# Kernel optimization log

Measured on AMD Instinct MI355X. Metric: run time of the kernel, lower is better.

The kernel has to match this reference:

```python
import jax, jax.numpy as jnp
import numpy as np

N = 8192
E = 262144


def gconv(x, e0, e1, W, b):
    # Dense symmetric adjacency with set-to-1 semantics (duplicates collapse),
    # matching adj[e0,e1]=1; adj[e1,e0]=1 in the original.
    n = x.shape[0]
    adj = jnp.zeros((n, n), x.dtype).at[e0, e1].set(1.0).at[e1, e0].set(1.0)
    adj = adj + jnp.eye(n, dtype=x.dtype)  # self-loops (selfloop=True branch)
    deg = jnp.sum(adj, axis=1)
    dinv = 1.0 / jnp.sqrt(deg)
    # D @ adj @ D expressed as row/col scaling (same math, no O(n^3) diag matmuls)
    adj = dinv[:, None] * adj * dinv[None, :]
    return adj @ (x @ W) + b


def setup_inputs() -> dict:
    key = jax.random.key(0)
    ks = jax.random.split(key, 8)
    x = jax.random.normal(ks[0], (N, 512), dtype=jnp.float32)
    edge_index = jax.random.randint(ks[1], (2, E), 0, N, dtype=jnp.int64)
    W1 = jax.random.normal(ks[2], (512, 512), dtype=jnp.float32)
    b1 = jnp.zeros((512,), dtype=jnp.float32)
    W2 = jax.random.normal(ks[3], (512, 512), dtype=jnp.float32)
    b2 = jnp.zeros((512,), dtype=jnp.float32)
    W3 = jax.random.normal(ks[4], (512, 256), dtype=jnp.float32)
    b3 = jnp.zeros((256,), dtype=jnp.float32)
    return {"x": x, "edge_index": edge_index, "W1": W1, "b1": b1,
            "W2": W2, "b2": b2, "W3": W3, "b3": b3}


def reference(x, edge_index, W1, b1, W2, b2, W3, b3):
    e0, e1 = edge_index[0], edge_index[1]
    # eval mode: dropout_edge / dropout are identity; norm=False so no PairNorm
    h = jax.nn.relu(gconv(x, e0, e1, W1, b1))   # conv1: inputs -> wide
    h = jax.nn.relu(gconv(h, e0, e1, W2, b2))   # conv2: blocks=3 -> one middle layer
    out = gconv(h, e0, e1, W3, b3)              # conv3: wide -> outputs
    return out
```

## Files before the change

### kernel.cpp

```cpp
#include <hip/hip_runtime.h>
#include <stdint.h>

#define NN 8192
#define WPR 256
#define CSTRIDE 192

typedef _Float16 f16;
typedef f16 f16x2 __attribute__((ext_vector_type(2)));
typedef f16 f16x4 __attribute__((ext_vector_type(4)));
typedef f16 f16x8 __attribute__((ext_vector_type(8)));
typedef float f32x4 __attribute__((ext_vector_type(4)));

__global__ __launch_bounds__(256) void build_adj(const int* __restrict__ ei,
                                                 uint32_t* __restrict__ mask,
                                                 int E) {
  int t = blockIdx.x * blockDim.x + threadIdx.x;
  if (t >= E) return;
  int a = ei[t];
  int b = ei[E + t];
  atomicOr(&mask[(size_t)a * WPR + (b >> 5)], 1u << (b & 31));
  atomicOr(&mask[(size_t)b * WPR + (a >> 5)], 1u << (a & 31));
}

__global__ __launch_bounds__(256) void mask_to_csr(const uint32_t* __restrict__ mask,
                                                   uint16_t* __restrict__ cols,
                                                   int* __restrict__ nnz,
                                                   float* __restrict__ dinv) {
  const int row = blockIdx.x * 4 + (threadIdx.x >> 6);
  const int lane = threadIdx.x & 63;
  const uint4 w = ((const uint4*)(mask + (size_t)row * WPR))[lane];
  const int c = __popc(w.x) + __popc(w.y) + __popc(w.z) + __popc(w.w);
  int inc = c;
#pragma unroll
  for (int o = 1; o < 64; o <<= 1) {
    int v = __shfl_up(inc, o);
    if (lane >= o) inc += v;
  }
  const int total = __shfl(inc, 63);
  int base = row * CSTRIDE + (inc - c);
  const int lim = row * CSTRIDE + CSTRIDE;
  uint32_t ws_[4] = {w.x, w.y, w.z, w.w};
#pragma unroll
  for (int i = 0; i < 4; ++i) {
    uint32_t word = ws_[i];
    int boff = (lane * 4 + i) << 5;
    while (word) {
      int b = __ffs(word) - 1;
      word &= word - 1;
      if (base < lim) cols[base] = (uint16_t)(boff + b);
      ++base;
    }
  }
  if (lane == 0) {
    nnz[row] = (total > CSTRIDE) ? CSTRIDE : total;
    dinv[row] = rsqrtf((float)(total + 1));
  }
}

__global__ __launch_bounds__(256) void wcvt_all(const float* __restrict__ W1,
                                                const float* __restrict__ W2,
                                                const float* __restrict__ W3,
                                                f16* __restrict__ T1,
                                                f16* __restrict__ T2,
                                                f16* __restrict__ T3) {
  int tile = blockIdx.x;
  const float* W; f16* T; int N;
  if (tile < 256)      { W = W1; T = T1; N = 512; }
  else if (tile < 512) { W = W2; T = T2; N = 512; tile -= 256; }
  else                 { W = W3; T = T3; N = 256; tile -= 512; }
  const int K = 512;
  const int ntn = N >> 5;
  const int k0 = (tile / ntn) << 5, n0 = (tile % ntn) << 5;
  __shared__ f16 tl[32][33];
  const int tx = threadIdx.x & 31, ty = threadIdx.x >> 5;
#pragma unroll
  for (int r = 0; r < 32; r += 8)
    tl[ty + r][tx] = (f16)W[(size_t)(k0 + ty + r) * N + n0 + tx];
  __syncthreads();
#pragma unroll
  for (int r = 0; r < 32; r += 8)
    T[(size_t)(n0 + ty + r) * K + k0 + tx] = tl[tx][ty + r];
}

template <typename AT>
__global__ __launch_bounds__(256) void gemm_f16(const AT* __restrict__ A,
                                                const f16* __restrict__ Wt,
                                                const float* __restrict__ rs,
                                                f16* __restrict__ Ys,
                                                int M, int N, int K) {
  __shared__ f16 As[128][40];
  __shared__ f16 Bs[64][40];
  const int t = threadIdx.x;
  const int lane = t & 63;
  const int w = t >> 6;
  const int wr = w >> 1, wc = w & 1;
  const int m0 = blockIdx.y * 128, n0 = blockIdx.x * 64;
  const int lm = lane & 15, kg = lane >> 4;
  const int k0f = kg * 8;

  f32x4 acc[4][2] = {};

  for (int k0 = 0; k0 < K; k0 += 32) {
    if constexpr (sizeof(AT) == 4) {
#pragma unroll
      for (int l = 0; l < 4; ++l) {
        int row = (t >> 3) + l * 32;
        int c4 = (t & 7) * 4;
        float4 v = *(const float4*)&A[(size_t)(m0 + row) * K + k0 + c4];
        f16x4 h = {(f16)v.x, (f16)v.y, (f16)v.z, (f16)v.w};
        *(f16x4*)&As[row][c4] = h;
      }
    } else {
#pragma unroll
      for (int l = 0; l < 2; ++l) {
        int idx = l * 256 + t;
        int row = idx >> 2;
        int c8 = (idx & 3) * 8;
        f16x8 h = *(const f16x8*)&A[(size_t)(m0 + row) * K + k0 + c8];
        *(f16x8*)&As[row][c8] = h;
      }
    }
    {
      int n = t >> 2, k8 = (t & 3) * 8;
      *(f16x8*)&Bs[n][k8] = *(const f16x8*)&Wt[(size_t)(n0 + n) * K + k0 + k8];
    }
    __syncthreads();

    f16x8 af[4], bf[2];
#pragma unroll
    for (int mf = 0; mf < 4; ++mf)
      af[mf] = *(const f16x8*)&As[wr * 64 + mf * 16 + lm][k0f];
#pragma unroll
    for (int nf = 0; nf < 2; ++nf)
      bf[nf] = *(const f16x8*)&Bs[wc * 32 + nf * 16 + lm][k0f];
#pragma unroll
    for (int mf = 0; mf < 4; ++mf)
#pragma unroll
      for (int nf = 0; nf < 2; ++nf)
        acc[mf][nf] = __builtin_amdgcn_mfma_f32_16x16x32_f16(af[mf], bf[nf], acc[mf][nf], 0, 0, 0);
    __syncthreads();
  }

#pragma unroll
  for (int mf = 0; mf < 4; ++mf) {
#pragma unroll
    for (int r = 0; r < 4; ++r) {
      int row = m0 + wr * 64 + mf * 16 + kg * 4 + r;
      float s = rs[row];
#pragma unroll
      for (int nf = 0; nf < 2; ++nf) {
        int col = n0 + wc * 32 + nf * 16 + lm;
        Ys[(size_t)row * N + col] = (f16)(s * acc[mf][nf][r]);
      }
    }
  }
}

template <int NC, typename OutT, bool RELU>
__global__ __launch_bounds__(256) void spmm_csr(const uint16_t* __restrict__ cols,
                                                const int* __restrict__ nnz,
                                                const float* __restrict__ dinv,
                                                const f16* __restrict__ Ys,
                                                const float* __restrict__ bias,
                                                OutT* __restrict__ out) {
  constexpr int Q = NC / 128;
  const int b = blockIdx.x;
  const int chunk = b % Q;
  const int rg = b / Q;
  const int w = threadIdx.x >> 6, lane = threadIdx.x & 63;
  const int row = rg * 4 + w;
  const int cb = chunk * 128 + 2 * lane;

  __shared__ uint16_t cidx[4][CSTRIDE];
  const int n = nnz[row];
  for (int k = lane; k < n; k += 64) cidx[w][k] = cols[row * CSTRIDE + k];
  __syncthreads();

  const f16* __restrict__ Yc = Ys + cb;
  float a0 = 0.f, a1 = 0.f;
  int k = 0;
  for (; k + 16 <= n; k += 16) {
    f16x2 v0  = *(const f16x2*)&Yc[(size_t)cidx[w][k + 0]  * NC];
    f16x2 v1  = *(const f16x2*)&Yc[(size_t)cidx[w][k + 1]  * NC];
    f16x2 v2  = *(const f16x2*)&Yc[(size_t)cidx[w][k + 2]  * NC];
    f16x2 v3  = *(const f16x2*)&Yc[(size_t)cidx[w][k + 3]  * NC];
    f16x2 v4  = *(const f16x2*)&Yc[(size_t)cidx[w][k + 4]  * NC];
    f16x2 v5  = *(const f16x2*)&Yc[(size_t)cidx[w][k + 5]  * NC];
    f16x2 v6  = *(const f16x2*)&Yc[(size_t)cidx[w][k + 6]  * NC];
    f16x2 v7  = *(const f16x2*)&Yc[(size_t)cidx[w][k + 7]  * NC];
    f16x2 v8  = *(const f16x2*)&Yc[(size_t)cidx[w][k + 8]  * NC];
    f16x2 v9  = *(const f16x2*)&Yc[(size_t)cidx[w][k + 9]  * NC];
    f16x2 v10 = *(const f16x2*)&Yc[(size_t)cidx[w][k + 10] * NC];
    f16x2 v11 = *(const f16x2*)&Yc[(size_t)cidx[w][k + 11] * NC];
    f16x2 v12 = *(const f16x2*)&Yc[(size_t)cidx[w][k + 12] * NC];
    f16x2 v13 = *(const f16x2*)&Yc[(size_t)cidx[w][k + 13] * NC];
    f16x2 v14 = *(const f16x2*)&Yc[(size_t)cidx[w][k + 14] * NC];
    f16x2 v15 = *(const f16x2*)&Yc[(size_t)cidx[w][k + 15] * NC];
    f16x2 s0 = ((v0 + v1) + (v2 + v3)) + ((v4 + v5) + (v6 + v7));
    f16x2 s1 = ((v8 + v9) + (v10 + v11)) + ((v12 + v13) + (v14 + v15));
    a0 += (float)s0[0] + (float)s1[0];
    a1 += (float)s0[1] + (float)s1[1];
  }
  for (; k + 8 <= n; k += 8) {
    f16x2 v0 = *(const f16x2*)&Yc[(size_t)cidx[w][k + 0] * NC];
    f16x2 v1 = *(const f16x2*)&Yc[(size_t)cidx[w][k + 1] * NC];
    f16x2 v2 = *(const f16x2*)&Yc[(size_t)cidx[w][k + 2] * NC];
    f16x2 v3 = *(const f16x2*)&Yc[(size_t)cidx[w][k + 3] * NC];
    f16x2 v4 = *(const f16x2*)&Yc[(size_t)cidx[w][k + 4] * NC];
    f16x2 v5 = *(const f16x2*)&Yc[(size_t)cidx[w][k + 5] * NC];
    f16x2 v6 = *(const f16x2*)&Yc[(size_t)cidx[w][k + 6] * NC];
    f16x2 v7 = *(const f16x2*)&Yc[(size_t)cidx[w][k + 7] * NC];
    f16x2 s = ((v0 + v1) + (v2 + v3)) + ((v4 + v5) + (v6 + v7));
    a0 += (float)s[0];
    a1 += (float)s[1];
  }
  for (; k < n; ++k) {
    f16x2 v = *(const f16x2*)&Yc[(size_t)cidx[w][k] * NC];
    a0 += (float)v[0]; a1 += (float)v[1];
  }
  f16x2 vs = *(const f16x2*)&Yc[(size_t)row * NC];
  a0 += (float)vs[0]; a1 += (float)vs[1];
  const float di = dinv[row];
  float o0 = di * a0 + bias[cb];
  float o1 = di * a1 + bias[cb + 1];
  if (RELU) { o0 = fmaxf(o0, 0.f); o1 = fmaxf(o1, 0.f); }
  if constexpr (sizeof(OutT) == 4) {
    *(float2*)&out[(size_t)row * NC + cb] = make_float2(o0, o1);
  } else {
    f16x2 h = {(f16)o0, (f16)o1};
    *(f16x2*)&out[(size_t)row * NC + cb] = h;
  }
}

extern "C" void kernel_launch(void* const* d_in, const int* in_sizes, int n_in,
                              void* d_out, int out_size, void* d_ws, size_t ws_size,
                              hipStream_t stream) {
  const float* x  = (const float*)d_in[0];
  const int*   ei = (const int*)d_in[1];
  const float* W1 = (const float*)d_in[2];
  const float* b1 = (const float*)d_in[3];
  const float* W2 = (const float*)d_in[4];
  const float* b2 = (const float*)d_in[5];
  const float* W3 = (const float*)d_in[6];
  const float* b3 = (const float*)d_in[7];
  float* out = (float*)d_out;
  const int E = in_sizes[1] / 2;

  uint8_t* ws = (uint8_t*)d_ws;
  size_t off = 0;
  uint16_t* cols = (uint16_t*)ws;            off += (size_t)CSTRIDE * NN * 2;
  int*      nnz  = (int*)(ws + off);         off += (size_t)NN * 4;
  float*    dinv = (float*)(ws + off);       off += (size_t)NN * 4;
  f16*      Wt1  = (f16*)(ws + off);         off += (size_t)512 * 512 * 2;
  f16*      Wt2  = (f16*)(ws + off);         off += (size_t)512 * 512 * 2;
  f16*      Wt3  = (f16*)(ws + off);         off += (size_t)256 * 512 * 2;
  f16*      H    = (f16*)(ws + off);         off += (size_t)NN * 512 * 2;
  f16*      Ys   = (f16*)(ws + off);
  uint32_t* mask = (uint32_t*)Ys;

  hipMemsetAsync(mask, 0, (size_t)NN * WPR * sizeof(uint32_t), stream);
  build_adj<<<(E + 255) / 256, 256, 0, stream>>>(ei, mask, E);
  mask_to_csr<<<NN / 4, 256, 0, stream>>>(mask, cols, nnz, dinv);
  wcvt_all<<<640, 256, 0, stream>>>(W1, W2, W3, Wt1, Wt2, Wt3);

  gemm_f16<float><<<dim3(8, 64), 256, 0, stream>>>(x, Wt1, dinv, Ys, NN, 512, 512);
  spmm_csr<512, f16, true><<<(NN / 4) * 4, 256, 0, stream>>>(cols, nnz, dinv, Ys, b1, H);

  gemm_f16<f16><<<dim3(8, 64), 256, 0, stream>>>(H, Wt2, dinv, Ys, NN, 512, 512);
  spmm_csr<512, f16, true><<<(NN / 4) * 4, 256, 0, stream>>>(cols, nnz, dinv, Ys, b2, H);

  gemm_f16<f16><<<dim3(4, 64), 256, 0, stream>>>(H, Wt3, dinv, Ys, NN, 256, 512);
  spmm_csr<256, float, false><<<(NN / 4) * 2, 256, 0, stream>>>(cols, nnz, dinv, Ys, b3, out);
}
```

Measured before the change: 223.2 us.

## Replace tiled GEMM with full-K panel GEMM and pre-convert x to fp16

The GEMM now loads a 32-row by full-K A panel into shared memory once, and each wave streams its slice of the transposed weights directly from global/L2 with no per-k-step barriers. Each block covers every output column, so A is read only once. The fp32 input x is converted to fp16 up front inside the weight-prep kernel, so all three GEMMs share one fp16 code path. The cost is an extra pass over x, 32KB of LDS per block, and B fragments that come from cache rather than shared memory. It also increases per-wave accumulator registers.

New measurement: 235.1 us. +5.3%, slower.

```diff
diff --git a/kernel.cpp b/kernel.cpp
--- a/kernel.cpp
+++ b/kernel.cpp
@@ -57,13 +57,24 @@
   }
 }
 
-__global__ __launch_bounds__(256) void wcvt_all(const float* __restrict__ W1,
+__global__ __launch_bounds__(256) void prep_all(const float* __restrict__ W1,
                                                 const float* __restrict__ W2,
                                                 const float* __restrict__ W3,
+                                                const float* __restrict__ x,
                                                 f16* __restrict__ T1,
                                                 f16* __restrict__ T2,
-                                                f16* __restrict__ T3) {
+                                                f16* __restrict__ T3,
+                                                f16* __restrict__ Xh) {
   int tile = blockIdx.x;
+  if (tile >= 640) {
+    size_t base = (size_t)(tile - 640) * 2048 + threadIdx.x * 8;
+    float4 v0 = *(const float4*)&x[base];
+    float4 v1 = *(const float4*)&x[base + 4];
+    f16x8 h = {(f16)v0.x, (f16)v0.y, (f16)v0.z, (f16)v0.w,
+               (f16)v1.x, (f16)v1.y, (f16)v1.z, (f16)v1.w};
+    *(f16x8*)&Xh[base] = h;
+    return;
+  }
   const float* W; f16* T; int N;
   if (tile < 256)      { W = W1; T = T1; N = 512; }
   else if (tile < 512) { W = W2; T = T2; N = 512; tile -= 256; }
@@ -82,74 +93,55 @@
     T[(size_t)(n0 + ty + r) * K + k0 + tx] = tl[tx][ty + r];
 }
 
-template <typename AT>
-__global__ __launch_bounds__(256) void gemm_f16(const AT* __restrict__ A,
-                                                const f16* __restrict__ Wt,
-                                                const float* __restrict__ rs,
-                                                f16* __restrict__ Ys,
-                                                int M, int N, int K) {
-  __shared__ f16 As[128][40];
-  __shared__ f16 Bs[64][40];
+template <int N>
+__global__ __launch_bounds__(256) void gemm_panel(const f16* __restrict__ A,
+                                                  const f16* __restrict__ Wt,
+                                                  const float* __restrict__ rs,
+                                                  f16* __restrict__ Ys) {
+  constexpr int K = 512;
+  constexpr int NF = N / 64;
+  __shared__ f16 As[32 * K];
   const int t = threadIdx.x;
   const int lane = t & 63;
   const int w = t >> 6;
-  const int wr = w >> 1, wc = w & 1;
-  const int m0 = blockIdx.y * 128, n0 = blockIdx.x * 64;
   const int lm = lane & 15, kg = lane >> 4;
-  const int k0f = kg * 8;
-
-  f32x4 acc[4][2] = {};
-
+  const int m0 = blockIdx.x * 32;
+  const int n0w = w * (N / 4);
+
+#pragma unroll
+  for (int i = 0; i < 8; ++i) {
+    int idx = i * 256 + t;
+    *(f16x8*)&As[idx * 8] = *(const f16x8*)&A[(size_t)m0 * K + idx * 8];
+  }
+  __syncthreads();
+
+  f32x4 acc[2][NF] = {};
+#pragma unroll 4
   for (int k0 = 0; k0 < K; k0 += 32) {
-    if constexpr (sizeof(AT) == 4) {
-#pragma unroll
-      for (int l = 0; l < 4; ++l) {
-        int row = (t >> 3) + l * 32;
-        int c4 = (t & 7) * 4;
-        float4 v = *(const float4*)&A[(size_t)(m0 + row) * K + k0 + c4];
-        f16x4 h = {(f16)v.x, (f16)v.y, (f16)v.z, (f16)v.w};
-        *(f16x4*)&As[row][c4] = h;
-      }
-    } else {
-#pragma unroll
-      for (int l = 0; l < 2; ++l) {
-        int idx = l * 256 + t;
-        int row = idx >> 2;
-        int c8 = (idx & 3) * 8;
-        f16x8 h = *(const f16x8*)&A[(size_t)(m0 + row) * K + k0 + c8];
-        *(f16x8*)&As[row][c8] = h;
-      }
-    }
-    {
-      int n = t >> 2, k8 = (t & 3) * 8;
-      *(f16x8*)&Bs[n][k8] = *(const f16x8*)&Wt[(size_t)(n0 + n) * K + k0 + k8];
-    }
-    __syncthreads();
-
-    f16x8 af[4], bf[2];
-#pragma unroll
-    for (int mf = 0; mf < 4; ++mf)
-      af[mf] = *(const f16x8*)&As[wr * 64 + mf * 16 + lm][k0f];
-#pragma unroll
-    for (int nf = 0; nf < 2; ++nf)
-      bf[nf] = *(const f16x8*)&Bs[wc * 32 + nf * 16 + lm][k0f];
-#pragma unroll
-    for (int mf = 0; mf < 4; ++mf)
-#pragma unroll
-      for (int nf = 0; nf < 2; ++nf)
+    f16x8 af[2];
+#pragma unroll
+    for (int mf = 0; mf < 2; ++mf)
+      af[mf] = *(const f16x8*)&As[(mf * 16 + lm) * K + k0 + kg * 8];
+    f16x8 bf[NF];
+#pragma unroll
+    for (int nf = 0; nf < NF; ++nf)
+      bf[nf] = *(const f16x8*)&Wt[(size_t)(n0w + nf * 16 + lm) * K + k0 + kg * 8];
+#pragma unroll
+    for (int mf = 0; mf < 2; ++mf)
+#pragma unroll
+      for (int nf = 0; nf < NF; ++nf)
         acc[mf][nf] = __builtin_amdgcn_mfma_f32_16x16x32_f16(af[mf], bf[nf], acc[mf][nf], 0, 0, 0);
-    __syncthreads();
-  }
-
-#pragma unroll
-  for (int mf = 0; mf < 4; ++mf) {
+  }
+
+#pragma unroll
+  for (int mf = 0; mf < 2; ++mf) {
 #pragma unroll
     for (int r = 0; r < 4; ++r) {
-      int row = m0 + wr * 64 + mf * 16 + kg * 4 + r;
+      int row = m0 + mf * 16 + kg * 4 + r;
       float s = rs[row];
 #pragma unroll
-      for (int nf = 0; nf < 2; ++nf) {
-        int col = n0 + wc * 32 + nf * 16 + lm;
+      for (int nf = 0; nf < NF; ++nf) {
+        int col = n0w + nf * 16 + lm;
         Ys[(size_t)row * N + col] = (f16)(s * acc[mf][nf][r]);
       }
     }
@@ -254,6 +246,7 @@
   f16*      Wt1  = (f16*)(ws + off);         off += (size_t)512 * 512 * 2;
   f16*      Wt2  = (f16*)(ws + off);         off += (size_t)512 * 512 * 2;
   f16*      Wt3  = (f16*)(ws + off);         off += (size_t)256 * 512 * 2;
+  f16*      Xh   = (f16*)(ws + off);         off += (size_t)NN * 512 * 2;
   f16*      H    = (f16*)(ws + off);         off += (size_t)NN * 512 * 2;
   f16*      Ys   = (f16*)(ws + off);
   uint32_t* mask = (uint32_t*)Ys;
@@ -261,14 +254,14 @@
   hipMemsetAsync(mask, 0, (size_t)NN * WPR * sizeof(uint32_t), stream);
   build_adj<<<(E + 255) / 256, 256, 0, stream>>>(ei, mask, E);
   mask_to_csr<<<NN / 4, 256, 0, stream>>>(mask, cols, nnz, dinv);
-  wcvt_all<<<640, 256, 0, stream>>>(W1, W2, W3, Wt1, Wt2, Wt3);
-
-  gemm_f16<float><<<dim3(8, 64), 256, 0, stream>>>(x, Wt1, dinv, Ys, NN, 512, 512);
+  prep_all<<<2688, 256, 0, stream>>>(W1, W2, W3, x, Wt1, Wt2, Wt3, Xh);
+
+  gemm_panel<512><<<NN / 32, 256, 0, stream>>>(Xh, Wt1, dinv, Ys);
   spmm_csr<512, f16, true><<<(NN / 4) * 4, 256, 0, stream>>>(cols, nnz, dinv, Ys, b1, H);
 
-  gemm_f16<f16><<<dim3(8, 64), 256, 0, stream>>>(H, Wt2, dinv, Ys, NN, 512, 512);
+  gemm_panel<512><<<NN / 32, 256, 0, stream>>>(H, Wt2, dinv, Ys);
   spmm_csr<512, f16, true><<<(NN / 4) * 4, 256, 0, stream>>>(cols, nnz, dinv, Ys, b2, H);
 
-  gemm_f16<f16><<<dim3(4, 64), 256, 0, stream>>>(H, Wt3, dinv, Ys, NN, 256, 512);
+  gemm_panel<256><<<NN / 32, 256, 0, stream>>>(H, Wt3, dinv, Ys);
   spmm_csr<256, float, false><<<(NN / 4) * 2, 256, 0, stream>>>(cols, nnz, dinv, Ys, b3, out);
 }
```
